# Optimization experiments

Hardware: AMD Instinct MI355X
Metric: run time of the kernel (lower is better)

## Reference

```python
import jax, jax.numpy as jnp
import numpy as np

B, C, H, W, Q = 4, 64, 128, 128, 30000
HID = 256
IN_DIM = C * 9 + 4  # unfolded feat + rel_coord(2) + rel_cell(2)


def setup_inputs() -> dict:
    key = jax.random.key(0)
    ks = jax.random.split(key, 14)
    inp = jax.random.normal(ks[0], (B, 1, H, W), jnp.float32)
    coord = jax.random.uniform(ks[1], (B, Q, 2), jnp.float32, -1.0, 1.0)
    cell = jnp.full((B, Q, 2), 2.0 / 256.0, jnp.float32)  # HR cell size for 256x256 target
    conv_w = jax.random.normal(ks[2], (C, 1, 3, 3), jnp.float32) * 0.3
    conv_b = jnp.zeros((C,), jnp.float32)
    def lin(k, fi, fo):
        return jax.random.normal(k, (fi, fo), jnp.float32) * (1.0 / np.sqrt(fi))
    w1 = lin(ks[3], IN_DIM, HID); b1 = jnp.zeros((HID,), jnp.float32)
    w2 = lin(ks[4], HID, HID);    b2 = jnp.zeros((HID,), jnp.float32)
    w3 = lin(ks[5], HID, HID);    b3 = jnp.zeros((HID,), jnp.float32)
    w4 = lin(ks[6], HID, HID);    b4 = jnp.zeros((HID,), jnp.float32)
    w5 = lin(ks[7], HID, 1);      b5 = jnp.zeros((1,), jnp.float32)
    return dict(inp=inp, coord=coord, cell=cell, conv_w=conv_w, conv_b=conv_b,
                w1=w1, b1=b1, w2=w2, b2=b2, w3=w3, b3=b3, w4=w4, b4=b4, w5=w5, b5=b5)


def _mlp(x, w1, b1, w2, b2, w3, b3, w4, b4, w5, b5):
    h = jax.nn.relu(x @ w1 + b1)
    h = jax.nn.relu(h @ w2 + b2)
    h = jax.nn.relu(h @ w3 + b3)
    h = jax.nn.relu(h @ w4 + b4)
    return h @ w5 + b5


def reference(inp, coord, cell, conv_w, conv_b, w1, b1, w2, b2, w3, b3, w4, b4, w5, b5):
    # encoder: conv3x3, pad 1 (NCHW)
    feat = jax.lax.conv_general_dilated(
        inp, conv_w, window_strides=(1, 1), padding=((1, 1), (1, 1)),
        dimension_numbers=("NCHW", "OIHW", "NCHW")) + conv_b[None, :, None, None]
    # feat_unfold: F.unfold(feat, 3, padding=1).view(B, C*9, H, W)
    pad = jnp.pad(feat, ((0, 0), (0, 0), (1, 1), (1, 1)))
    patches = jnp.stack([pad[:, :, kh:kh + H, kw:kw + W]
                         for kh in range(3) for kw in range(3)], axis=2)  # (B,C,9,H,W)
    featu = patches.reshape(B, C * 9, H, W)
    featu_t = featu.transpose(0, 2, 3, 1).reshape(B, H * W, C * 9)  # (B,HW,Cu)

    rx = 1.0 / H  # 2/H/2
    ry = 1.0 / W
    eps_shift = 1e-6
    Hf = jnp.float32(H); Wf = jnp.float32(W)
    rel_cell = cell * jnp.array([H, W], jnp.float32)  # same for all branches

    preds, areas = [], []
    for vx in (-1.0, 1.0):
        for vy in (-1.0, 1.0):
            c0 = jnp.clip(coord[..., 0] + vx * rx + eps_shift, -1 + 1e-6, 1 - 1e-6)
            c1 = jnp.clip(coord[..., 1] + vy * ry + eps_shift, -1 + 1e-6, 1 - 1e-6)
            # nearest grid_sample, align_corners=False (round half-to-even = nearbyint)
            i = jnp.clip(jnp.round((c0 + 1.0) * Hf / 2.0 - 0.5), 0.0, Hf - 1.0)
            j = jnp.clip(jnp.round((c1 + 1.0) * Wf / 2.0 - 0.5), 0.0, Wf - 1.0)
            # q_coord = feat_coord sampled at same nearest index (pixel centers)
            qy = -1.0 + (2.0 * i + 1.0) / Hf
            qx = -1.0 + (2.0 * j + 1.0) / Wf
            idx = (i * Wf + j).astype(jnp.int32)  # (B,Q)
            q_feat = jnp.take_along_axis(featu_t, idx[..., None], axis=1)  # (B,Q,Cu)
            rel0 = (coord[..., 0] - qy) * Hf
            rel1 = (coord[..., 1] - qx) * Wf
            x = jnp.concatenate([q_feat, rel0[..., None], rel1[..., None], rel_cell], axis=-1)
            pred = _mlp(x.reshape(B * Q, -1), w1, b1, w2, b2, w3, b3, w4, b4, w5, b5)
            preds.append(pred.reshape(B, Q, -1))
            areas.append(jnp.abs(rel0 * rel1) + 1e-9)

    tot_area = areas[0] + areas[1] + areas[2] + areas[3]
    # local_ensemble: swap diagonally-opposite areas
    areas = [areas[3], areas[2], areas[1], areas[0]]
    ret = jnp.zeros_like(preds[0])
    for pred, area in zip(preds, areas):
        ret = ret + pred * (area / tot_area)[..., None]
    return ret  # (B, Q, 1)
```

## Files before the change

kernel.cpp:

```cpp
#include <hip/hip_runtime.h>
#include <stdint.h>


typedef unsigned short u16;
typedef __attribute__((ext_vector_type(8))) short   short8;
typedef __attribute__((ext_vector_type(8))) __bf16  bf16x8;
typedef __attribute__((ext_vector_type(4))) float   f32x4;

__device__ __forceinline__ float bf2f(u16 u) {
  union { uint32_t i; float f; } v; v.i = ((uint32_t)u) << 16; return v.f;
}
__device__ __forceinline__ u16 f2bf(float f) {
  union { float f; uint32_t i; } v; v.f = f;
  return (u16)((v.i + 0x7FFFu + ((v.i >> 16) & 1u)) >> 16);
}
__device__ __forceinline__ u16 bfbits(float f) {
  union { __bf16 h; u16 u; } c; c.h = (__bf16)f; return c.u;
}

__global__ void prep_weights(const float* __restrict__ w1, const float* __restrict__ w2,
                             const float* __restrict__ w3, const float* __restrict__ w4,
                             const float* __restrict__ cw, const float* __restrict__ cb,
                             u16* __restrict__ W2t, u16* __restrict__ w2t,
                             u16* __restrict__ w3t, u16* __restrict__ w4t) {
  int tid = blockIdx.x * 256 + threadIdx.x;
  if (tid < 24576) {
    int o = tid / 96, k = tid - o * 96;
    float s = 0.0f;
    if (k < 90) {
      int t = k / 10, j = k - t * 10;
      if (j == 9) {
        for (int c = 0; c < 64; ++c) s += cb[c] * w1[(c * 9 + t) * 256 + o];
      } else {
        for (int c = 0; c < 64; ++c) s += cw[c * 9 + j] * w1[(c * 9 + t) * 256 + o];
      }
    }
    W2t[o * 96 + k] = f2bf(s);
  } else {
    int u = tid - 24576;
    if (u < 3 * 65536) {
      int layer = u >> 16, r = u & 65535;
      int o = r >> 8, k = r & 255;
      const float* src = (layer == 0) ? w2 : (layer == 1) ? w3 : w4;
      u16* dst = (layer == 0) ? w2t : (layer == 1) ? w3t : w4t;
      dst[o * 256 + k] = f2bf(src[k * 256 + o]);
    }
  }
}

__global__ __launch_bounds__(256) void h1pre_kernel(const float* __restrict__ inp,
                                                    const u16* __restrict__ W2t,
                                                    const float* __restrict__ b1,
                                                    u16* __restrict__ h1pre) {
  __shared__ short Al[64 * 120];

  int tid = threadIdx.x;
  int lane = tid & 63, wave = tid >> 6;
  int g = lane >> 4, l15 = lane & 15;
  int wc0 = wave * 64;
  int bid = blockIdx.x;
  int b = bid >> 8, rem = bid & 255;
  int y = rem >> 1, x0 = (rem & 1) << 6;

  {
    int px = tid >> 2, q = tid & 3;
    int x = x0 + px;
    const float* ip = inp + b * 16384;
    #pragma unroll
    for (int c8 = 0; c8 < 3; ++c8) {
      short8 av;
      #pragma unroll
      for (int e = 0; e < 8; ++e) {
        int k = q * 24 + c8 * 8 + e;
        float val = 0.0f;
        if (k < 90) {
          int t = k / 10, j = k - t * 10;
          int dh = t / 3 - 1, dw = t % 3 - 1;
          int yy = y + dh, xx = x + dw;
          bool m = (yy >= 0) && (yy < 128) && (xx >= 0) && (xx < 128);
          if (j == 9) {
            val = m ? 1.0f : 0.0f;
          } else {
            int sh = j / 3 - 1, sw = j % 3 - 1;
            int r = yy + sh, c = xx + sw;
            val = (m && r >= 0 && r < 128 && c >= 0 && c < 128) ? ip[r * 128 + c] : 0.0f;
          }
        }
        av[e] = (short)f2bf(val);
      }
      *(short8*)(&Al[px * 120 + q * 24 + c8 * 8]) = av;
    }
  }
  __syncthreads();

  bf16x8 breg[12];
  #pragma unroll
  for (int ks = 0; ks < 3; ++ks)
    #pragma unroll
    for (int nf = 0; nf < 4; ++nf)
      breg[ks * 4 + nf] =
          *(const bf16x8*)(W2t + (wc0 + nf * 16 + l15) * 96 + ks * 32 + g * 8);

  f32x4 acc[4][4];
  #pragma unroll
  for (int mf = 0; mf < 4; ++mf)
    #pragma unroll
    for (int nf = 0; nf < 4; ++nf) acc[mf][nf] = (f32x4){0.f, 0.f, 0.f, 0.f};

  #pragma unroll
  for (int ks = 0; ks < 3; ++ks) {
    bf16x8 a[4];
    #pragma unroll
    for (int mf = 0; mf < 4; ++mf)
      a[mf] = *(const bf16x8*)(&Al[(mf * 16 + l15) * 120 + ks * 32 + g * 8]);
    #pragma unroll
    for (int nf = 0; nf < 4; ++nf)
      #pragma unroll
      for (int mf = 0; mf < 4; ++mf)
        acc[mf][nf] = __builtin_amdgcn_mfma_f32_16x16x32_bf16(
            breg[ks * 4 + nf], a[mf], acc[mf][nf], 0, 0, 0);
  }

  #pragma unroll
  for (int nf = 0; nf < 4; ++nf) {
    int o0 = wc0 + nf * 16 + 4 * g;
    f32x4 bv = *(const f32x4*)(b1 + o0);
    #pragma unroll
    for (int mf = 0; mf < 4; ++mf) {
      int pixel = y * 128 + x0 + mf * 16 + l15;
      u16 p0 = f2bf(acc[mf][nf][0] + bv[0]);
      u16 p1 = f2bf(acc[mf][nf][1] + bv[1]);
      u16 p2 = f2bf(acc[mf][nf][2] + bv[2]);
      u16 p3 = f2bf(acc[mf][nf][3] + bv[3]);
      unsigned long long w =
          (unsigned long long)(p0 | ((uint32_t)p1 << 16)) |
          ((unsigned long long)(p2 | ((uint32_t)p3 << 16)) << 32);
      *(unsigned long long*)(h1pre + (((size_t)((b << 14) + pixel)) << 8) + o0) = w;
    }
  }
}

__global__ __launch_bounds__(256, 2) void mlp_kernel(
    const float* __restrict__ coord, const float* __restrict__ cell,
    const u16* __restrict__ h1pre,
    const u16* __restrict__ w2t, const u16* __restrict__ w3t, const u16* __restrict__ w4t,
    const float* __restrict__ w1, const float* __restrict__ b2, const float* __restrict__ b3,
    const float* __restrict__ b4, const float* __restrict__ w5, const float* __restrict__ b5,
    float* __restrict__ out) {
  __shared__ short Xl[2][64 * 256];
  __shared__ float relv[128][4];
  __shared__ float area_l[128];
  __shared__ int   idx_l[128];
  __shared__ float predp[4][128];

  int tid = threadIdx.x;
  int lane = tid & 63, wave = tid >> 6;
  int g = lane >> 4, l15 = lane & 15;
  int wc0 = wave * 64;
  int xr = l15 & 7;
  int bid = blockIdx.x;

  int c16 = tid & 31;
  float wrr[4][8];
  {
    const float* wr = w1 + 576 * 256;
    #pragma unroll
    for (int a = 0; a < 4; ++a) {
      f32x4 u0 = *(const f32x4*)(wr + a * 256 + c16 * 8);
      f32x4 u1 = *(const f32x4*)(wr + a * 256 + c16 * 8 + 4);
      #pragma unroll
      for (int e = 0; e < 4; ++e) { wrr[a][e] = u0[e]; wrr[a][4 + e] = u1[e]; }
    }
  }

  if (tid < 128) {
    int t = tid >> 2, br = tid & 3;
    int gq = bid * 32 + t;
    int b = gq / 30000;
    float c0 = coord[gq * 2 + 0];
    float c1 = coord[gq * 2 + 1];
    float ce0 = cell[gq * 2 + 0];
    float ce1 = cell[gq * 2 + 1];
    float vx = (br & 2) ? 1.0f : -1.0f;
    float vy = (br & 1) ? 1.0f : -1.0f;
    float s0 = c0 + vx * (1.0f / 128.0f) + 1e-6f;
    float s1 = c1 + vy * (1.0f / 128.0f) + 1e-6f;
    s0 = fminf(fmaxf(s0, -1.0f + 1e-6f), 1.0f - 1e-6f);
    s1 = fminf(fmaxf(s1, -1.0f + 1e-6f), 1.0f - 1e-6f);
    float fi = rintf((s0 + 1.0f) * 64.0f - 0.5f);
    float fj = rintf((s1 + 1.0f) * 64.0f - 0.5f);
    fi = fminf(fmaxf(fi, 0.0f), 127.0f);
    fj = fminf(fmaxf(fj, 0.0f), 127.0f);
    float qy = -1.0f + (2.0f * fi + 1.0f) / 128.0f;
    float qx = -1.0f + (2.0f * fj + 1.0f) / 128.0f;
    float rel0 = (c0 - qy) * 128.0f;
    float rel1 = (c1 - qx) * 128.0f;
    idx_l[tid] = (b << 14) + (int)fi * 128 + (int)fj;
    relv[tid][0] = rel0;
    relv[tid][1] = rel1;
    relv[tid][2] = ce0 * 128.0f;
    relv[tid][3] = ce1 * 128.0f;
    area_l[tid] = fabsf(rel0 * rel1) + 1e-9f;
  }
  __syncthreads();

  {
    short8 v[16];
    #pragma unroll
    for (int it = 0; it < 8; ++it) {
      int rl = it * 8 + (tid >> 5);
      v[it]     = *(const short8*)(h1pre + ((size_t)idx_l[rl] << 8) + c16 * 8);
      v[8 + it] = *(const short8*)(h1pre + ((size_t)idx_l[64 + rl] << 8) + c16 * 8);
    }
    __builtin_amdgcn_sched_barrier(0);
    #pragma unroll
    for (int t = 0; t < 2; ++t) {
      #pragma unroll
      for (int it = 0; it < 8; ++it) {
        int rl = it * 8 + (tid >> 5);
        int row = t * 64 + rl;
        float r0 = relv[row][0], r1 = relv[row][1], r2 = relv[row][2], r3 = relv[row][3];
        short8 xo;
        #pragma unroll
        for (int e = 0; e < 8; ++e) {
          float val = bf2f((u16)v[t * 8 + it][e]) + r0 * wrr[0][e] + r1 * wrr[1][e] +
                      r2 * wrr[2][e] + r3 * wrr[3][e];
          xo[e] = (short)bfbits(fmaxf(val, 0.0f));
        }
        *(short8*)(&Xl[t][rl * 256 + ((c16 ^ (rl & 7)) * 8)]) = xo;
      }
    }
  }
  __syncthreads();

  const u16* Wgs[3] = {w2t, w3t, w4t};
  const float* Bgs[3] = {b2, b3, b4};

  #pragma unroll
  for (int layer = 0; layer < 3; ++layer) {
    const u16* Wg = Wgs[layer];
    const float* bias = Bgs[layer];

    bf16x8 breg[32];
    #pragma unroll
    for (int ks = 0; ks < 8; ++ks)
      #pragma unroll
      for (int nf = 0; nf < 4; ++nf)
        breg[ks * 4 + nf] =
            *(const bf16x8*)(Wg + (wc0 + nf * 16 + l15) * 256 + ks * 32 + g * 8);
    __builtin_amdgcn_sched_barrier(0);

    #pragma unroll
    for (int t = 0; t < 2; ++t) {
      f32x4 acc[4][4];
      #pragma unroll
      for (int mf = 0; mf < 4; ++mf)
        #pragma unroll
        for (int nf = 0; nf < 4; ++nf) acc[mf][nf] = (f32x4){0.f, 0.f, 0.f, 0.f};

      #pragma unroll
      for (int ks = 0; ks < 8; ++ks) {
        bf16x8 a[4];
        #pragma unroll
        for (int mf = 0; mf < 4; ++mf)
          a[mf] = *(const bf16x8*)(&Xl[t][(mf * 16 + l15) * 256 + (((ks * 4 + g) ^ xr) * 8)]);
        #pragma unroll
        for (int nf = 0; nf < 4; ++nf)
          #pragma unroll
          for (int mf = 0; mf < 4; ++mf)
            acc[mf][nf] = __builtin_amdgcn_mfma_f32_16x16x32_bf16(
                breg[ks * 4 + nf], a[mf], acc[mf][nf], 0, 0, 0);
      }

      __syncthreads();
      if (layer < 2) {
        #pragma unroll
        for (int nf = 0; nf < 4; ++nf) {
          int o0 = wc0 + nf * 16 + 4 * g;
          f32x4 bv = *(const f32x4*)(bias + o0);
          #pragma unroll
          for (int mf = 0; mf < 4; ++mf) {
            u16 p0 = bfbits(fmaxf(acc[mf][nf][0] + bv[0], 0.0f));
            u16 p1 = bfbits(fmaxf(acc[mf][nf][1] + bv[1], 0.0f));
            u16 p2 = bfbits(fmaxf(acc[mf][nf][2] + bv[2], 0.0f));
            u16 p3 = bfbits(fmaxf(acc[mf][nf][3] + bv[3], 0.0f));
            unsigned long long w =
                (unsigned long long)(p0 | ((uint32_t)p1 << 16)) |
                ((unsigned long long)(p2 | ((uint32_t)p3 << 16)) << 32);
            int idx = (mf * 16 + l15) * 256 + (((o0 >> 3) ^ xr) * 8) + (o0 & 7);
            *(unsigned long long*)(&Xl[t][idx]) = w;
          }
        }
      } else {
        float s[4] = {0.f, 0.f, 0.f, 0.f};
        #pragma unroll
        for (int nf = 0; nf < 4; ++nf) {
          int o0 = wc0 + nf * 16 + 4 * g;
          f32x4 bv = *(const f32x4*)(b4 + o0);
          f32x4 wv = *(const f32x4*)(w5 + o0);
          #pragma unroll
          for (int mf = 0; mf < 4; ++mf)
            #pragma unroll
            for (int i = 0; i < 4; ++i)
              s[mf] += fmaxf(acc[mf][nf][i] + bv[i], 0.0f) * wv[i];
        }
        #pragma unroll
        for (int mf = 0; mf < 4; ++mf) {
          s[mf] += __shfl_xor(s[mf], 16, 64);
          s[mf] += __shfl_xor(s[mf], 32, 64);
        }
        if (lane < 16) {
          #pragma unroll
          for (int mf = 0; mf < 4; ++mf)
            predp[wave][t * 64 + mf * 16 + lane] = s[mf];
        }
      }
    }
    __syncthreads();
  }

  if (tid < 32) {
    int gq = bid * 32 + tid;
    float pr[4], ar[4];
    #pragma unroll
    for (int br = 0; br < 4; ++br) {
      int r = tid * 4 + br;
      pr[br] = predp[0][r] + predp[1][r] + predp[2][r] + predp[3][r] + b5[0];
      ar[br] = area_l[r];
    }
    float tot = ar[0] + ar[1] + ar[2] + ar[3];
    float ret = 0.0f;
    #pragma unroll
    for (int br = 0; br < 4; ++br) ret += pr[br] * (ar[3 - br] / tot);
    out[gq] = ret;
  }
}

extern "C" void kernel_launch(void* const* d_in, const int* in_sizes, int n_in,
                              void* d_out, int out_size, void* d_ws, size_t ws_size,
                              hipStream_t stream) {
  const float* inp    = (const float*)d_in[0];
  const float* coord  = (const float*)d_in[1];
  const float* cell   = (const float*)d_in[2];
  const float* conv_w = (const float*)d_in[3];
  const float* conv_b = (const float*)d_in[4];
  const float* w1 = (const float*)d_in[5];
  const float* b1 = (const float*)d_in[6];
  const float* w2 = (const float*)d_in[7];
  const float* b2 = (const float*)d_in[8];
  const float* w3 = (const float*)d_in[9];
  const float* b3 = (const float*)d_in[10];
  const float* w4 = (const float*)d_in[11];
  const float* b4 = (const float*)d_in[12];
  const float* w5 = (const float*)d_in[13];
  const float* b5 = (const float*)d_in[14];
  float* out = (float*)d_out;

  char* ws = (char*)d_ws;
  u16* h1pre = (u16*)(ws);
  u16* W2t   = (u16*)(ws + 33554432);
  u16* w2t   = (u16*)(ws + 33603584);
  u16* w3t   = (u16*)(ws + 33734656);
  u16* w4t   = (u16*)(ws + 33865728);

  hipLaunchKernelGGL(prep_weights, dim3(864), dim3(256), 0, stream,
                     w1, w2, w3, w4, conv_w, conv_b, W2t, w2t, w3t, w4t);
  hipLaunchKernelGGL(h1pre_kernel, dim3(1024), dim3(256), 0, stream,
                     inp, W2t, b1, h1pre);
  hipLaunchKernelGGL(mlp_kernel, dim3(3750), dim3(256), 0, stream,
                     coord, cell, h1pre, w2t, w3t, w4t, w1, b2, b3, b4, w5, b5, out);
}
```

Before: 310.7 us.

## Switch MLP layers from 16x16x32 to 32x32x16 bf16 MFMA tiles

Replaces the 16x16x32 MFMA tiling (4x4 fragments per wave) with 32x32x16 MFMA tiling (2x2 fragments of 16 accumulators each) for the three hidden 256x256 layers. The LDS swizzle is widened from 8 to 16 slots to match the new row access pattern, and the epilogue and final reduction are remapped to the 32x32 output layout. This halves the number of A-fragment LDS reads per k-step and uses the larger MFMA shape, at the cost of a different register layout and possible LDS bank-conflict changes.

```diff
diff --git a/kernel.cpp b/kernel.cpp
--- a/kernel.cpp
+++ b/kernel.cpp
@@ -3,9 +3,10 @@
 
 
 typedef unsigned short u16;
-typedef __attribute__((ext_vector_type(8))) short   short8;
-typedef __attribute__((ext_vector_type(8))) __bf16  bf16x8;
-typedef __attribute__((ext_vector_type(4))) float   f32x4;
+typedef __attribute__((ext_vector_type(8)))  short   short8;
+typedef __attribute__((ext_vector_type(8)))  __bf16  bf16x8;
+typedef __attribute__((ext_vector_type(4)))  float   f32x4;
+typedef __attribute__((ext_vector_type(16))) float   f32x16;
 
 __device__ __forceinline__ float bf2f(u16 u) {
   union { uint32_t i; float f; } v; v.i = ((uint32_t)u) << 16; return v.f;
@@ -155,9 +156,8 @@
 
   int tid = threadIdx.x;
   int lane = tid & 63, wave = tid >> 6;
-  int g = lane >> 4, l15 = lane & 15;
+  int l31 = lane & 31, h = lane >> 5;
   int wc0 = wave * 64;
-  int xr = l15 & 7;
   int bid = blockIdx.x;
 
   int c16 = tid & 31;
@@ -227,7 +227,7 @@
                       r2 * wrr[2][e] + r3 * wrr[3][e];
           xo[e] = (short)bfbits(fmaxf(val, 0.0f));
         }
-        *(short8*)(&Xl[t][rl * 256 + ((c16 ^ (rl & 7)) * 8)]) = xo;
+        *(short8*)(&Xl[t][rl * 256 + ((c16 ^ (rl & 15)) * 8)]) = xo;
       }
     }
   }
@@ -243,76 +243,85 @@
 
     bf16x8 breg[32];
     #pragma unroll
-    for (int ks = 0; ks < 8; ++ks)
-      #pragma unroll
-      for (int nf = 0; nf < 4; ++nf)
-        breg[ks * 4 + nf] =
-            *(const bf16x8*)(Wg + (wc0 + nf * 16 + l15) * 256 + ks * 32 + g * 8);
+    for (int ks = 0; ks < 16; ++ks)
+      #pragma unroll
+      for (int nf = 0; nf < 2; ++nf)
+        breg[ks * 2 + nf] =
+            *(const bf16x8*)(Wg + (wc0 + nf * 32 + l31) * 256 + ks * 16 + h * 8);
     __builtin_amdgcn_sched_barrier(0);
 
     #pragma unroll
     for (int t = 0; t < 2; ++t) {
-      f32x4 acc[4][4];
-      #pragma unroll
-      for (int mf = 0; mf < 4; ++mf)
-        #pragma unroll
-        for (int nf = 0; nf < 4; ++nf) acc[mf][nf] = (f32x4){0.f, 0.f, 0.f, 0.f};
-
-      #pragma unroll
-      for (int ks = 0; ks < 8; ++ks) {
-        bf16x8 a[4];
-        #pragma unroll
-        for (int mf = 0; mf < 4; ++mf)
-          a[mf] = *(const bf16x8*)(&Xl[t][(mf * 16 + l15) * 256 + (((ks * 4 + g) ^ xr) * 8)]);
-        #pragma unroll
-        for (int nf = 0; nf < 4; ++nf)
-          #pragma unroll
-          for (int mf = 0; mf < 4; ++mf)
-            acc[mf][nf] = __builtin_amdgcn_mfma_f32_16x16x32_bf16(
-                breg[ks * 4 + nf], a[mf], acc[mf][nf], 0, 0, 0);
+      f32x16 acc[2][2];
+      #pragma unroll
+      for (int mf = 0; mf < 2; ++mf)
+        #pragma unroll
+        for (int nf = 0; nf < 2; ++nf)
+          #pragma unroll
+          for (int i = 0; i < 16; ++i) acc[mf][nf][i] = 0.f;
+
+      #pragma unroll
+      for (int ks = 0; ks < 16; ++ks) {
+        bf16x8 a[2];
+        #pragma unroll
+        for (int mf = 0; mf < 2; ++mf) {
+          int q = mf * 32 + l31;
+          int slot = (ks * 2 + h) ^ (q & 15);
+          a[mf] = *(const bf16x8*)(&Xl[t][q * 256 + slot * 8]);
+        }
+        #pragma unroll
+        for (int nf = 0; nf < 2; ++nf)
+          #pragma unroll
+          for (int mf = 0; mf < 2; ++mf)
+            acc[mf][nf] = __builtin_amdgcn_mfma_f32_32x32x16_bf16(
+                breg[ks * 2 + nf], a[mf], acc[mf][nf], 0, 0, 0);
       }
 
       __syncthreads();
       if (layer < 2) {
         #pragma unroll
-        for (int nf = 0; nf < 4; ++nf) {
-          int o0 = wc0 + nf * 16 + 4 * g;
-          f32x4 bv = *(const f32x4*)(bias + o0);
-          #pragma unroll
-          for (int mf = 0; mf < 4; ++mf) {
-            u16 p0 = bfbits(fmaxf(acc[mf][nf][0] + bv[0], 0.0f));
-            u16 p1 = bfbits(fmaxf(acc[mf][nf][1] + bv[1], 0.0f));
-            u16 p2 = bfbits(fmaxf(acc[mf][nf][2] + bv[2], 0.0f));
-            u16 p3 = bfbits(fmaxf(acc[mf][nf][3] + bv[3], 0.0f));
-            unsigned long long w =
-                (unsigned long long)(p0 | ((uint32_t)p1 << 16)) |
-                ((unsigned long long)(p2 | ((uint32_t)p3 << 16)) << 32);
-            int idx = (mf * 16 + l15) * 256 + (((o0 >> 3) ^ xr) * 8) + (o0 & 7);
-            *(unsigned long long*)(&Xl[t][idx]) = w;
+        for (int nf = 0; nf < 2; ++nf) {
+          #pragma unroll
+          for (int j = 0; j < 4; ++j) {
+            int o0 = wc0 + nf * 32 + 8 * j + 4 * h;
+            f32x4 bv = *(const f32x4*)(bias + o0);
+            #pragma unroll
+            for (int mf = 0; mf < 2; ++mf) {
+              int q = mf * 32 + l31;
+              u16 p0 = bfbits(fmaxf(acc[mf][nf][4 * j + 0] + bv[0], 0.0f));
+              u16 p1 = bfbits(fmaxf(acc[mf][nf][4 * j + 1] + bv[1], 0.0f));
+              u16 p2 = bfbits(fmaxf(acc[mf][nf][4 * j + 2] + bv[2], 0.0f));
+              u16 p3 = bfbits(fmaxf(acc[mf][nf][4 * j + 3] + bv[3], 0.0f));
+              unsigned long long w =
+                  (unsigned long long)(p0 | ((uint32_t)p1 << 16)) |
+                  ((unsigned long long)(p2 | ((uint32_t)p3 << 16)) << 32);
+              int idx = q * 256 + (((o0 >> 3) ^ (q & 15)) * 8) + (o0 & 7);
+              *(unsigned long long*)(&Xl[t][idx]) = w;
+            }
           }
         }
       } else {
-        float s[4] = {0.f, 0.f, 0.f, 0.f};
-        #pragma unroll
-        for (int nf = 0; nf < 4; ++nf) {
-          int o0 = wc0 + nf * 16 + 4 * g;
-          f32x4 bv = *(const f32x4*)(b4 + o0);
-          f32x4 wv = *(const f32x4*)(w5 + o0);
-          #pragma unroll
-          for (int mf = 0; mf < 4; ++mf)
+        float s[2] = {0.f, 0.f};
+        #pragma unroll
+        for (int nf = 0; nf < 2; ++nf) {
+          #pragma unroll
+          for (int j = 0; j < 4; ++j) {
+            int o0 = wc0 + nf * 32 + 8 * j + 4 * h;
+            f32x4 bv = *(const f32x4*)(b4 + o0);
+            f32x4 wv = *(const f32x4*)(w5 + o0);
             #pragma unroll
-            for (int i = 0; i < 4; ++i)
-              s[mf] += fmaxf(acc[mf][nf][i] + bv[i], 0.0f) * wv[i];
-        }
-        #pragma unroll
-        for (int mf = 0; mf < 4; ++mf) {
-          s[mf] += __shfl_xor(s[mf], 16, 64);
-          s[mf] += __shfl_xor(s[mf], 32, 64);
-        }
-        if (lane < 16) {
-          #pragma unroll
-          for (int mf = 0; mf < 4; ++mf)
-            predp[wave][t * 64 + mf * 16 + lane] = s[mf];
+            for (int mf = 0; mf < 2; ++mf)
+              #pragma unroll
+              for (int i = 0; i < 4; ++i)
+                s[mf] += fmaxf(acc[mf][nf][4 * j + i] + bv[i], 0.0f) * wv[i];
+          }
+        }
+        #pragma unroll
+        for (int mf = 0; mf < 2; ++mf) s[mf] += __shfl_xor(s[mf], 32, 64);
+        if (lane < 32) {
+          #pragma unroll
+          for (int mf = 0; mf < 2; ++mf)
+            predp[wave][t * 64 + mf * 32 + l31] = s[mf];
         }
       }
     }
```

Result: slower. 327.6 us (+5.4%).
